# Kernel tuning notes

Measured on AMD Instinct MI355X. Metric: run time of the kernel, lower is better.

Reference implementation:

```python
import jax, jax.numpy as jnp
import numpy as np

IGNORE_INDEX = -100
LABEL_SMOOTHING = 0.0
BT, H, V = 4096, 2048, 32000


def setup_inputs() -> dict:
    key = jax.random.key(0)
    k1, k2, k3, k4 = jax.random.split(key, 4)
    x = jax.random.normal(k1, (BT, H), dtype=jnp.float32)
    target = jax.random.randint(k2, (BT,), 0, V, dtype=jnp.int64)
    weight = jax.random.normal(k3, (V, H), dtype=jnp.float32) * 0.02
    bias = jax.random.normal(k4, (V,), dtype=jnp.float32) * 0.02
    return {"x": x, "target": target, "weight": weight, "bias": bias}


def reference(x, target, weight, bias):
    # logits: [BT, V] — the module avoids materializing this by chunking;
    # as a correctness reference we compute it directly.
    logits = jnp.einsum('th,vh->tv', x, weight) + bias
    lse = jax.nn.logsumexp(logits, axis=-1)                      # [BT]
    tgt_logit = jnp.take_along_axis(logits, target[:, None], axis=-1)[:, 0]
    valid = target != IGNORE_INDEX
    total = jnp.maximum(valid.sum(), 1).astype(logits.dtype)
    per_tok = -(tgt_logit - lse)                                 # hard-label NLL
    if LABEL_SMOOTHING > 0.0:
        eps = LABEL_SMOOTHING / V
        per_tok = per_tok * (1.0 - LABEL_SMOOTHING) + (
            -eps * logits.sum(axis=-1) + LABEL_SMOOTHING * lse)
    per_tok = jnp.where(valid, per_tok, 0.0)
    # reduction == 'mean': divide by number of non-ignored targets
    loss = per_tok.sum() / total
    return loss
```

## Files before the change

kernel.cpp:

```cpp
#include <hip/hip_runtime.h>
#include <hip/hip_bf16.h>
#include <cstdint>

#define BT 4096
#define H  2048
#define V  32000
#define TM 128
#define TN 128
#define BK 128
#define NVT (V/TN)
#define NRT (BT/TM)
#define PJ  256
#define WSCALE 64.0f
#define INV_WSCALE 0.015625f

typedef int   v8i   __attribute__((ext_vector_type(8)));
typedef float f32x4 __attribute__((ext_vector_type(4)));

__device__ __forceinline__ void async_load16(const void* g, void* l) {
    __builtin_amdgcn_global_load_lds(
        (__attribute__((address_space(1))) uint32_t*)(void*)g,
        (__attribute__((address_space(3))) uint32_t*)l, 16, 0, 0);
}

__global__ void quant_all(const float4* __restrict__ X4, const float4* __restrict__ W4,
                          int* __restrict__ Xq, int* __restrict__ Wq,
                          float* __restrict__ accum) {
    const int NX = BT * H / 4;
    const int NW = (int)((size_t)V * H / 4);
    int i = blockIdx.x * blockDim.x + threadIdx.x;
    if (i == 0) { accum[0] = 0.f; accum[1] = 0.f; }
    if (i < NX) {
        float4 v = X4[i];
        int p = __builtin_amdgcn_cvt_pk_fp8_f32(v.x, v.y, 0, false);
        p     = __builtin_amdgcn_cvt_pk_fp8_f32(v.z, v.w, p, true);
        Xq[i] = p;
    } else if (i < NX + NW) {
        int j = i - NX;
        float4 v = W4[j];
        int p = __builtin_amdgcn_cvt_pk_fp8_f32(v.x * WSCALE, v.y * WSCALE, 0, false);
        p     = __builtin_amdgcn_cvt_pk_fp8_f32(v.z * WSCALE, v.w * WSCALE, p, true);
        Wq[j] = p;
    }
}

__global__ __launch_bounds__(256, 3) void gemm_lse(
    const uint8_t* __restrict__ Xq,
    const uint8_t* __restrict__ Wq,
    const float* __restrict__ bias,
    const int*  __restrict__ target,
    float* __restrict__ part_m,
    float* __restrict__ part_l,
    float* __restrict__ tgt_logit)
{
    __shared__ __align__(16) uint8_t As[TM * BK];
    __shared__ __align__(16) uint8_t Bs[TN * BK];
    __shared__ float red_m[2][TM];
    __shared__ float red_l[2][TM];
    __shared__ int   tgts[TM];

    const int tid  = threadIdx.x;
    const int lane = tid & 63;
    const int wave = tid >> 6;
    const int wm   = wave >> 1;
    const int wn   = wave & 1;
    const int row0 = blockIdx.x * TM;
    const int col0 = blockIdx.y * TN;

    if (tid < TM) tgts[tid] = target[row0 + tid];

    f32x4 acc[4][4];
#pragma unroll
    for (int i = 0; i < 4; i++)
#pragma unroll
        for (int j = 0; j < 4; j++) acc[i][j] = (f32x4){0.f, 0.f, 0.f, 0.f};

    const int srow   = lane >> 3;
    const int schunk = ((lane & 7) ^ srow) * 16;

    const uint8_t* Aptr = Xq + (size_t)row0 * H + (size_t)(wave * 32 + srow) * H + schunk;
    const uint8_t* Bptr = Wq + (size_t)col0 * H + (size_t)(wave * 32 + srow) * H + schunk;

    const int lr  = lane & 15;
    const int g32 = lane >> 4;

    for (int k0 = 0; k0 < H; k0 += BK) {
#pragma unroll
        for (int L = 0; L < 4; L++) {
            const int g = wave * 4 + L;
            async_load16(Aptr + (size_t)(8 * L) * H, &As[g * 1024]);
            async_load16(Bptr + (size_t)(8 * L) * H, &Bs[g * 1024]);
        }
        Aptr += BK;
        Bptr += BK;
        __syncthreads();

        union Frag { int4 q[2]; v8i v; };
        Frag af[4], bf[4];
#pragma unroll
        for (int i = 0; i < 4; i++) {
            const int r  = wm * 64 + i * 16 + lr;
            const int p0 = (2 * g32) ^ (r & 7);
            const int4* base = (const int4*)&As[r * BK];
            af[i].q[0] = base[p0];
            af[i].q[1] = base[p0 ^ 1];
        }
#pragma unroll
        for (int j = 0; j < 4; j++) {
            const int r  = wn * 64 + j * 16 + lr;
            const int p0 = (2 * g32) ^ (r & 7);
            const int4* base = (const int4*)&Bs[r * BK];
            bf[j].q[0] = base[p0];
            bf[j].q[1] = base[p0 ^ 1];
        }
#pragma unroll
        for (int i = 0; i < 4; i++)
#pragma unroll
            for (int j = 0; j < 4; j++)
                acc[i][j] = __builtin_amdgcn_mfma_scale_f32_16x16x128_f8f6f4(
                    af[i].v, bf[j].v, acc[i][j],
                    0 , 0 ,
                    0, 0x7f7f7f7f, 0, 0x7f7f7f7f);
        __syncthreads();
    }

    const int quad = lane >> 4;
    float bj[4];
#pragma unroll
    for (int j = 0; j < 4; j++) bj[j] = bias[col0 + wn * 64 + j * 16 + lr];

#pragma unroll
    for (int i = 0; i < 4; i++) {
#pragma unroll
        for (int r = 0; r < 4; r++) {
            const int rit = wm * 64 + i * 16 + quad * 4 + r;
            float v[4];
#pragma unroll
            for (int j = 0; j < 4; j++) v[j] = acc[i][j][r] * INV_WSCALE + bj[j];
            const int tg = tgts[rit];
#pragma unroll
            for (int j = 0; j < 4; j++)
                if (col0 + wn * 64 + j * 16 + lr == tg)
                    tgt_logit[row0 + rit] = v[j];
            float mx = fmaxf(fmaxf(v[0], v[1]), fmaxf(v[2], v[3]));
#pragma unroll
            for (int d = 1; d < 16; d <<= 1) mx = fmaxf(mx, __shfl_xor(mx, d));
            float se = __expf(v[0] - mx) + __expf(v[1] - mx) +
                       __expf(v[2] - mx) + __expf(v[3] - mx);
#pragma unroll
            for (int d = 1; d < 16; d <<= 1) se += __shfl_xor(se, d);
            if (lr == 0) { red_m[wn][rit] = mx; red_l[wn][rit] = se; }
        }
    }
    __syncthreads();
    if (tid < TM) {
        float m0 = red_m[0][tid], m1 = red_m[1][tid];
        float l0 = red_l[0][tid], l1 = red_l[1][tid];
        float M = fmaxf(m0, m1);
        float L = l0 * __expf(m0 - M) + l1 * __expf(m1 - M);
        part_m[(size_t)(row0 + tid) * PJ + blockIdx.y] = M;
        part_l[(size_t)(row0 + tid) * PJ + blockIdx.y] = L;
    }
}

__global__ void finalize(const float* __restrict__ part_m,
                         const float* __restrict__ part_l,
                         const float* __restrict__ tgt_logit,
                         const int*  __restrict__ target,
                         float* __restrict__ accum)
{
    const int wave = threadIdx.x >> 6, lane = threadIdx.x & 63;
    const int t = blockIdx.x * 4 + wave;
    float m[4], l[4];
#pragma unroll
    for (int c = 0; c < 4; c++) {
        const int j = c * 64 + lane;
        const bool ok = j < NVT;
        m[c] = ok ? part_m[(size_t)t * PJ + j] : -1e30f;
        l[c] = ok ? part_l[(size_t)t * PJ + j] : 0.f;
    }
    float M = fmaxf(fmaxf(m[0], m[1]), fmaxf(m[2], m[3]));
#pragma unroll
    for (int d = 1; d < 64; d <<= 1) M = fmaxf(M, __shfl_xor(M, d));
    float S = l[0] * __expf(m[0] - M) + l[1] * __expf(m[1] - M) +
              l[2] * __expf(m[2] - M) + l[3] * __expf(m[3] - M);
#pragma unroll
    for (int d = 1; d < 64; d <<= 1) S += __shfl_xor(S, d);

    __shared__ float sm[4], sc[4];
    if (lane == 0) {
        const int tg = target[t];
        float loss = 0.f, cnt = 0.f;
        if (tg != -100) {
            loss = (M + __logf(S)) - tgt_logit[t];
            cnt  = 1.f;
        }
        sm[wave] = loss; sc[wave] = cnt;
    }
    __syncthreads();
    if (threadIdx.x == 0) {
        float Ls = sm[0] + sm[1] + sm[2] + sm[3];
        float Cs = sc[0] + sc[1] + sc[2] + sc[3];
        atomicAdd(&accum[0], Ls);
        atomicAdd(&accum[1], Cs);
    }
}

__global__ void final_div(const float* __restrict__ accum, float* __restrict__ out) {
    out[0] = accum[0] / fmaxf(accum[1], 1.f);
}

extern "C" void kernel_launch(void* const* d_in, const int* in_sizes, int n_in,
                              void* d_out, int out_size, void* d_ws, size_t ws_size,
                              hipStream_t stream) {
    const float* x      = (const float*)d_in[0];
    const int*   target = (const int*)d_in[1];
    const float* w      = (const float*)d_in[2];
    const float* bias   = (const float*)d_in[3];

    char* ws = (char*)d_ws;
    size_t off = 0;
    auto alloc = [&](size_t bytes) {
        void* p = ws + off;
        off += (bytes + 255) & ~(size_t)255;
        return p;
    };
    uint8_t* Xq   = (uint8_t*)alloc((size_t)BT * H);
    uint8_t* Wq   = (uint8_t*)alloc((size_t)V * H);
    float* part_m = (float*)alloc((size_t)BT * PJ * 4);
    float* part_l = (float*)alloc((size_t)BT * PJ * 4);
    float* tgtl   = (float*)alloc((size_t)BT * 4);
    float* accum  = (float*)alloc(256);

    const int nq = BT * H / 4 + (int)((size_t)V * H / 4);
    quant_all<<<(nq + 255) / 256, 256, 0, stream>>>(
        (const float4*)x, (const float4*)w, (int*)Xq, (int*)Wq, accum);

    dim3 grid(NRT, NVT);
    gemm_lse<<<grid, 256, 0, stream>>>(Xq, Wq, bias, target, part_m, part_l, tgtl);

    finalize<<<BT / 4, 256, 0, stream>>>(part_m, part_l, tgtl, target, accum);
    final_div<<<1, 1, 0, stream>>>(accum, (float*)d_out);
}
```

Baseline: 714.6 us.

## Enlarge GEMM tiles to 256x256 with double-buffered LDS and block swizzle

The fused GEMM+LSE kernel moves from 128x128 tiles with 4 waves to 256x256 tiles with 8 waves, double-buffered 128KB LDS staging, and a remapped 1D grid so neighbouring blocks share row tiles for better L2 reuse. Each wave now holds 8x4 MFMA accumulators, loads A fragments per row-slice, and raises wave priority around its MFMA bursts. Partial max/sum arrays shrink to 125 column blocks, and the quantize kernel uses nontemporal loads. The goal is more operand reuse and less global traffic per MFMA, at the cost of higher register and LDS pressure, which limits occupancy to one block per CU.

Measured after the change: 739.3 us. 1.03x slower.

```diff
diff --git a/kernel.cpp b/kernel.cpp
--- a/kernel.cpp
+++ b/kernel.cpp
@@ -1,21 +1,21 @@
 #include <hip/hip_runtime.h>
-#include <hip/hip_bf16.h>
 #include <cstdint>
 
 #define BT 4096
 #define H  2048
 #define V  32000
-#define TM 128
-#define TN 128
+#define BM 256
+#define BN 256
 #define BK 128
-#define NVT (V/TN)
-#define NRT (BT/TM)
-#define PJ  256
+#define NRT (BT/BM)
+#define NVT (V/BN)
+#define PJ  128
 #define WSCALE 64.0f
 #define INV_WSCALE 0.015625f
 
 typedef int   v8i   __attribute__((ext_vector_type(8)));
 typedef float f32x4 __attribute__((ext_vector_type(4)));
+typedef float f4v   __attribute__((ext_vector_type(4)));
 
 __device__ __forceinline__ void async_load16(const void* g, void* l) {
     __builtin_amdgcn_global_load_lds(
@@ -23,7 +23,7 @@
         (__attribute__((address_space(3))) uint32_t*)l, 16, 0, 0);
 }
 
-__global__ void quant_all(const float4* __restrict__ X4, const float4* __restrict__ W4,
+__global__ void quant_all(const float* __restrict__ X, const float* __restrict__ W,
                           int* __restrict__ Xq, int* __restrict__ Wq,
                           float* __restrict__ accum) {
     const int NX = BT * H / 4;
@@ -31,20 +31,20 @@
     int i = blockIdx.x * blockDim.x + threadIdx.x;
     if (i == 0) { accum[0] = 0.f; accum[1] = 0.f; }
     if (i < NX) {
-        float4 v = X4[i];
+        f4v v = __builtin_nontemporal_load((const f4v*)X + i);
         int p = __builtin_amdgcn_cvt_pk_fp8_f32(v.x, v.y, 0, false);
         p     = __builtin_amdgcn_cvt_pk_fp8_f32(v.z, v.w, p, true);
         Xq[i] = p;
     } else if (i < NX + NW) {
         int j = i - NX;
-        float4 v = W4[j];
+        f4v v = __builtin_nontemporal_load((const f4v*)W + j);
         int p = __builtin_amdgcn_cvt_pk_fp8_f32(v.x * WSCALE, v.y * WSCALE, 0, false);
         p     = __builtin_amdgcn_cvt_pk_fp8_f32(v.z * WSCALE, v.w * WSCALE, p, true);
         Wq[j] = p;
     }
 }
 
-__global__ __launch_bounds__(256, 3) void gemm_lse(
+__global__ __launch_bounds__(512, 2) void gemm_lse(
     const uint8_t* __restrict__ Xq,
     const uint8_t* __restrict__ Wq,
     const float* __restrict__ bias,
@@ -53,58 +53,59 @@
     float* __restrict__ part_l,
     float* __restrict__ tgt_logit)
 {
-    __shared__ __align__(16) uint8_t As[TM * BK];
-    __shared__ __align__(16) uint8_t Bs[TN * BK];
-    __shared__ float red_m[2][TM];
-    __shared__ float red_l[2][TM];
-    __shared__ int   tgts[TM];
+    __shared__ __align__(16) uint8_t smem[131072];
 
     const int tid  = threadIdx.x;
     const int lane = tid & 63;
     const int wave = tid >> 6;
-    const int wm   = wave >> 1;
-    const int wn   = wave & 1;
-    const int row0 = blockIdx.x * TM;
-    const int col0 = blockIdx.y * TN;
-
-    if (tid < TM) tgts[tid] = target[row0 + tid];
-
-    f32x4 acc[4][4];
-#pragma unroll
-    for (int i = 0; i < 4; i++)
+    const int wm   = wave >> 2;
+    const int wn   = wave & 3;
+
+    const int bid = blockIdx.x;
+    const int swz = (bid & 7) * 250 + (bid >> 3);
+    const int rbk = swz & 15;
+    const int cbk = swz >> 4;
+    const int row0 = rbk * BM;
+    const int col0 = cbk * BN;
+
+    f32x4 acc[8][4];
+#pragma unroll
+    for (int i = 0; i < 8; i++)
 #pragma unroll
         for (int j = 0; j < 4; j++) acc[i][j] = (f32x4){0.f, 0.f, 0.f, 0.f};
 
     const int srow   = lane >> 3;
     const int schunk = ((lane & 7) ^ srow) * 16;
-
-    const uint8_t* Aptr = Xq + (size_t)row0 * H + (size_t)(wave * 32 + srow) * H + schunk;
-    const uint8_t* Bptr = Wq + (size_t)col0 * H + (size_t)(wave * 32 + srow) * H + schunk;
+    const uint8_t* Aptr = Xq + (size_t)(row0 + 32 * wave + srow) * H + schunk;
+    const uint8_t* Bptr = Wq + (size_t)(col0 + 32 * wave + srow) * H + schunk;
+
+    auto stage = [&](int buf, const uint8_t* ap_, const uint8_t* bp_) {
+        uint8_t* as_ = smem + buf * 65536;
+        uint8_t* bs_ = smem + buf * 65536 + 32768;
+#pragma unroll
+        for (int L = 0; L < 4; L++) {
+            const int g = 4 * wave + L;
+            async_load16(ap_ + (size_t)(8 * L) * H, as_ + g * 1024);
+            async_load16(bp_ + (size_t)(8 * L) * H, bs_ + g * 1024);
+        }
+    };
+
+    stage(0, Aptr, Bptr);
+    __syncthreads();
 
     const int lr  = lane & 15;
     const int g32 = lane >> 4;
 
-    for (int k0 = 0; k0 < H; k0 += BK) {
-#pragma unroll
-        for (int L = 0; L < 4; L++) {
-            const int g = wave * 4 + L;
-            async_load16(Aptr + (size_t)(8 * L) * H, &As[g * 1024]);
-            async_load16(Bptr + (size_t)(8 * L) * H, &Bs[g * 1024]);
-        }
-        Aptr += BK;
-        Bptr += BK;
-        __syncthreads();
-
+    for (int t = 0; t < H / BK; ++t) {
+        const int cur = t & 1;
+        if (t < H / BK - 1) {
+            Aptr += BK; Bptr += BK;
+            stage(cur ^ 1, Aptr, Bptr);
+        }
+        const uint8_t* As = smem + cur * 65536;
+        const uint8_t* Bs = smem + cur * 65536 + 32768;
         union Frag { int4 q[2]; v8i v; };
-        Frag af[4], bf[4];
-#pragma unroll
-        for (int i = 0; i < 4; i++) {
-            const int r  = wm * 64 + i * 16 + lr;
-            const int p0 = (2 * g32) ^ (r & 7);
-            const int4* base = (const int4*)&As[r * BK];
-            af[i].q[0] = base[p0];
-            af[i].q[1] = base[p0 ^ 1];
-        }
+        Frag bf[4];
 #pragma unroll
         for (int j = 0; j < 4; j++) {
             const int r  = wn * 64 + j * 16 + lr;
@@ -114,15 +115,31 @@
             bf[j].q[1] = base[p0 ^ 1];
         }
 #pragma unroll
-        for (int i = 0; i < 4; i++)
+        for (int i = 0; i < 8; i++) {
+            const int r  = wm * 128 + i * 16 + lr;
+            const int p0 = (2 * g32) ^ (r & 7);
+            const int4* base = (const int4*)&As[r * BK];
+            Frag af;
+            af.q[0] = base[p0];
+            af.q[1] = base[p0 ^ 1];
+            __builtin_amdgcn_s_setprio(1);
 #pragma unroll
             for (int j = 0; j < 4; j++)
                 acc[i][j] = __builtin_amdgcn_mfma_scale_f32_16x16x128_f8f6f4(
-                    af[i].v, bf[j].v, acc[i][j],
+                    af.v, bf[j].v, acc[i][j],
                     0 , 0 ,
                     0, 0x7f7f7f7f, 0, 0x7f7f7f7f);
+            __builtin_amdgcn_s_setprio(0);
+        }
         __syncthreads();
     }
+
+    float* red_m = (float*)smem;
+    float* red_l = (float*)(smem + 4096);
+    int*   tgts  = (int*)(smem + 8192);
+
+    if (tid < 256) tgts[tid] = target[row0 + tid];
+    __syncthreads();
 
     const int quad = lane >> 4;
     float bj[4];
@@ -130,10 +147,10 @@
     for (int j = 0; j < 4; j++) bj[j] = bias[col0 + wn * 64 + j * 16 + lr];
 
 #pragma unroll
-    for (int i = 0; i < 4; i++) {
+    for (int i = 0; i < 8; i++) {
 #pragma unroll
         for (int r = 0; r < 4; r++) {
-            const int rit = wm * 64 + i * 16 + quad * 4 + r;
+            const int rit = wm * 128 + i * 16 + quad * 4 + r;
             float v[4];
 #pragma unroll
             for (int j = 0; j < 4; j++) v[j] = acc[i][j][r] * INV_WSCALE + bj[j];
@@ -149,17 +166,20 @@
                        __expf(v[2] - mx) + __expf(v[3] - mx);
 #pragma unroll
             for (int d = 1; d < 16; d <<= 1) se += __shfl_xor(se, d);
-            if (lr == 0) { red_m[wn][rit] = mx; red_l[wn][rit] = se; }
-        }
-    }
-    __syncthreads();
-    if (tid < TM) {
-        float m0 = red_m[0][tid], m1 = red_m[1][tid];
-        float l0 = red_l[0][tid], l1 = red_l[1][tid];
-        float M = fmaxf(m0, m1);
-        float L = l0 * __expf(m0 - M) + l1 * __expf(m1 - M);
-        part_m[(size_t)(row0 + tid) * PJ + blockIdx.y] = M;
-        part_l[(size_t)(row0 + tid) * PJ + blockIdx.y] = L;
+            if (lr == 0) { red_m[wn * 256 + rit] = mx; red_l[wn * 256 + rit] = se; }
+        }
+    }
+    __syncthreads();
+    if (tid < 256) {
+        float M = red_m[tid];
+        float m1 = red_m[256 + tid], m2 = red_m[512 + tid], m3 = red_m[768 + tid];
+        M = fmaxf(fmaxf(M, m1), fmaxf(m2, m3));
+        float L = red_l[tid]       * __expf(red_m[tid]       - M)
+                + red_l[256 + tid] * __expf(m1 - M)
+                + red_l[512 + tid] * __expf(m2 - M)
+                + red_l[768 + tid] * __expf(m3 - M);
+        part_m[(size_t)(row0 + tid) * PJ + cbk] = M;
+        part_l[(size_t)(row0 + tid) * PJ + cbk] = L;
     }
 }
 
@@ -171,19 +191,18 @@
 {
     const int wave = threadIdx.x >> 6, lane = threadIdx.x & 63;
     const int t = blockIdx.x * 4 + wave;
-    float m[4], l[4];
-#pragma unroll
-    for (int c = 0; c < 4; c++) {
+    float m[2], l[2];
+#pragma unroll
+    for (int c = 0; c < 2; c++) {
         const int j = c * 64 + lane;
         const bool ok = j < NVT;
         m[c] = ok ? part_m[(size_t)t * PJ + j] : -1e30f;
         l[c] = ok ? part_l[(size_t)t * PJ + j] : 0.f;
     }
-    float M = fmaxf(fmaxf(m[0], m[1]), fmaxf(m[2], m[3]));
+    float M = fmaxf(m[0], m[1]);
 #pragma unroll
     for (int d = 1; d < 64; d <<= 1) M = fmaxf(M, __shfl_xor(M, d));
-    float S = l[0] * __expf(m[0] - M) + l[1] * __expf(m[1] - M) +
-              l[2] * __expf(m[2] - M) + l[3] * __expf(m[3] - M);
+    float S = l[0] * __expf(m[0] - M) + l[1] * __expf(m[1] - M);
 #pragma unroll
     for (int d = 1; d < 64; d <<= 1) S += __shfl_xor(S, d);
 
@@ -234,11 +253,11 @@
 
     const int nq = BT * H / 4 + (int)((size_t)V * H / 4);
     quant_all<<<(nq + 255) / 256, 256, 0, stream>>>(
-        (const float4*)x, (const float4*)w, (int*)Xq, (int*)Wq, accum);
-
-    dim3 grid(NRT, NVT);
-    gemm_lse<<<grid, 256, 0, stream>>>(Xq, Wq, bias, target, part_m, part_l, tgtl);
+        x, w, (int*)Xq, (int*)Wq, accum);
+
+    gemm_lse<<<NRT * NVT, 512, 0, stream>>>(Xq, Wq, bias, target, part_m, part_l, tgtl);
 
     finalize<<<BT / 4, 256, 0, stream>>>(part_m, part_l, tgtl, target, accum);
+
     final_div<<<1, 1, 0, stream>>>(accum, (float*)d_out);
 }
```

## Double-buffer A tile in LDS, load B fragments directly to registers

Applied to the files above, without the earlier changes.

The GEMM main loop now double-buffers the X tile in shared memory and prefetches the next tile while computing the current one. The weight tile no longer goes through LDS: each lane reads its fragment straight from global memory into registers, one step ahead. The MFMA sections are wrapped in s_setprio, and the quantization kernel uses nontemporal loads. The aim is to hide global-load latency and halve the barriers per K step. The cost is more VGPR pressure under launch_bounds(256,3), and B reads from global are uncoalesced 32-byte row segments that rely on the cache.

Result: slower. 1.425 ms (+99.5%).

```diff
diff --git a/kernel.cpp b/kernel.cpp
--- a/kernel.cpp
+++ b/kernel.cpp
@@ -1,5 +1,4 @@
 #include <hip/hip_runtime.h>
-#include <hip/hip_bf16.h>
 #include <cstdint>
 
 #define BT 4096
@@ -8,14 +7,16 @@
 #define TM 128
 #define TN 128
 #define BK 128
+#define NT (H/BK)
+#define NRT (BT/TM)
 #define NVT (V/TN)
-#define NRT (BT/TM)
 #define PJ  256
 #define WSCALE 64.0f
 #define INV_WSCALE 0.015625f
 
 typedef int   v8i   __attribute__((ext_vector_type(8)));
 typedef float f32x4 __attribute__((ext_vector_type(4)));
+typedef float f4v   __attribute__((ext_vector_type(4)));
 
 __device__ __forceinline__ void async_load16(const void* g, void* l) {
     __builtin_amdgcn_global_load_lds(
@@ -23,7 +24,7 @@
         (__attribute__((address_space(3))) uint32_t*)l, 16, 0, 0);
 }
 
-__global__ void quant_all(const float4* __restrict__ X4, const float4* __restrict__ W4,
+__global__ void quant_all(const float* __restrict__ X, const float* __restrict__ W,
                           int* __restrict__ Xq, int* __restrict__ Wq,
                           float* __restrict__ accum) {
     const int NX = BT * H / 4;
@@ -31,13 +32,13 @@
     int i = blockIdx.x * blockDim.x + threadIdx.x;
     if (i == 0) { accum[0] = 0.f; accum[1] = 0.f; }
     if (i < NX) {
-        float4 v = X4[i];
+        f4v v = __builtin_nontemporal_load((const f4v*)X + i);
         int p = __builtin_amdgcn_cvt_pk_fp8_f32(v.x, v.y, 0, false);
         p     = __builtin_amdgcn_cvt_pk_fp8_f32(v.z, v.w, p, true);
         Xq[i] = p;
     } else if (i < NX + NW) {
         int j = i - NX;
-        float4 v = W4[j];
+        f4v v = __builtin_nontemporal_load((const f4v*)W + j);
         int p = __builtin_amdgcn_cvt_pk_fp8_f32(v.x * WSCALE, v.y * WSCALE, 0, false);
         p     = __builtin_amdgcn_cvt_pk_fp8_f32(v.z * WSCALE, v.w * WSCALE, p, true);
         Wq[j] = p;
@@ -53,8 +54,7 @@
     float* __restrict__ part_l,
     float* __restrict__ tgt_logit)
 {
-    __shared__ __align__(16) uint8_t As[TM * BK];
-    __shared__ __align__(16) uint8_t Bs[TN * BK];
+    __shared__ __align__(16) uint8_t As[2][TM * BK];
     __shared__ float red_m[2][TM];
     __shared__ float red_l[2][TM];
     __shared__ int   tgts[TM];
@@ -77,50 +77,76 @@
 
     const int srow   = lane >> 3;
     const int schunk = ((lane & 7) ^ srow) * 16;
-
-    const uint8_t* Aptr = Xq + (size_t)row0 * H + (size_t)(wave * 32 + srow) * H + schunk;
-    const uint8_t* Bptr = Wq + (size_t)col0 * H + (size_t)(wave * 32 + srow) * H + schunk;
+    const uint8_t* Aptr = Xq + (size_t)(row0 + wave * 32 + srow) * H + schunk;
 
     const int lr  = lane & 15;
     const int g32 = lane >> 4;
 
-    for (int k0 = 0; k0 < H; k0 += BK) {
-#pragma unroll
-        for (int L = 0; L < 4; L++) {
-            const int g = wave * 4 + L;
-            async_load16(Aptr + (size_t)(8 * L) * H, &As[g * 1024]);
-            async_load16(Bptr + (size_t)(8 * L) * H, &Bs[g * 1024]);
-        }
-        Aptr += BK;
-        Bptr += BK;
-        __syncthreads();
-
-        union Frag { int4 q[2]; v8i v; };
-        Frag af[4], bf[4];
-#pragma unroll
-        for (int i = 0; i < 4; i++) {
-            const int r  = wm * 64 + i * 16 + lr;
-            const int p0 = (2 * g32) ^ (r & 7);
-            const int4* base = (const int4*)&As[r * BK];
-            af[i].q[0] = base[p0];
-            af[i].q[1] = base[p0 ^ 1];
-        }
+    const uint8_t* Bbase = Wq + (size_t)(col0 + wn * 64 + lr) * H + g32 * 32;
+
+    union Frag { int4 q[2]; v8i v; };
+
+    auto stageA = [&](int buf) {
+#pragma unroll
+        for (int L = 0; L < 4; L++)
+            async_load16(Aptr + (size_t)(8 * L) * H, &As[buf][(wave * 4 + L) * 1024]);
+    };
+    auto loadB = [&](Frag* b, int k) {
 #pragma unroll
         for (int j = 0; j < 4; j++) {
-            const int r  = wn * 64 + j * 16 + lr;
-            const int p0 = (2 * g32) ^ (r & 7);
-            const int4* base = (const int4*)&Bs[r * BK];
-            bf[j].q[0] = base[p0];
-            bf[j].q[1] = base[p0 ^ 1];
-        }
-#pragma unroll
-        for (int i = 0; i < 4; i++)
+            const uint8_t* bp = Bbase + (size_t)(j * 16) * H + k;
+            b[j].q[0] = *(const int4*)(bp);
+            b[j].q[1] = *(const int4*)(bp + 16);
+        }
+    };
+    auto compute = [&](const uint8_t* As_, Frag* b) {
+#pragma unroll
+        for (int q = 0; q < 2; q++) {
+            Frag a0, a1;
+            {
+                const int r0 = wm * 64 + (2 * q) * 16 + lr;
+                const int p0 = (2 * g32) ^ (r0 & 7);
+                const int4* base0 = (const int4*)&As_[r0 * BK];
+                a0.q[0] = base0[p0];
+                a0.q[1] = base0[p0 ^ 1];
+                const int r1 = wm * 64 + (2 * q + 1) * 16 + lr;
+                const int p1 = (2 * g32) ^ (r1 & 7);
+                const int4* base1 = (const int4*)&As_[r1 * BK];
+                a1.q[0] = base1[p1];
+                a1.q[1] = base1[p1 ^ 1];
+            }
+            __builtin_amdgcn_s_setprio(1);
 #pragma unroll
             for (int j = 0; j < 4; j++)
-                acc[i][j] = __builtin_amdgcn_mfma_scale_f32_16x16x128_f8f6f4(
-                    af[i].v, bf[j].v, acc[i][j],
+                acc[2 * q][j] = __builtin_amdgcn_mfma_scale_f32_16x16x128_f8f6f4(
+                    a0.v, b[j].v, acc[2 * q][j],
                     0 , 0 ,
                     0, 0x7f7f7f7f, 0, 0x7f7f7f7f);
+#pragma unroll
+            for (int j = 0; j < 4; j++)
+                acc[2 * q + 1][j] = __builtin_amdgcn_mfma_scale_f32_16x16x128_f8f6f4(
+                    a1.v, b[j].v, acc[2 * q + 1][j],
+                    0, 0, 0, 0x7f7f7f7f, 0, 0x7f7f7f7f);
+            __builtin_amdgcn_s_setprio(0);
+        }
+    };
+
+    Frag bA[4], bB[4];
+
+    stageA(0); Aptr += BK;
+    loadB(bA, 0);
+    __syncthreads();
+
+    for (int tt = 0; tt < NT; tt += 2) {
+        stageA(1); Aptr += BK;
+        loadB(bB, (tt + 1) * BK);
+        compute(As[0], bA);
+        __syncthreads();
+        if (tt + 2 < NT) {
+            stageA(0); Aptr += BK;
+            loadB(bA, (tt + 2) * BK);
+        }
+        compute(As[1], bB);
         __syncthreads();
     }
 
@@ -234,11 +260,12 @@
 
     const int nq = BT * H / 4 + (int)((size_t)V * H / 4);
     quant_all<<<(nq + 255) / 256, 256, 0, stream>>>(
-        (const float4*)x, (const float4*)w, (int*)Xq, (int*)Wq, accum);
+        x, w, (int*)Xq, (int*)Wq, accum);
 
     dim3 grid(NRT, NVT);
     gemm_lse<<<grid, 256, 0, stream>>>(Xq, Wq, bias, target, part_m, part_l, tgtl);
 
     finalize<<<BT / 4, 256, 0, stream>>>(part_m, part_l, tgtl, target, accum);
+
     final_div<<<1, 1, 0, stream>>>(accum, (float*)d_out);
 }
```
